# Optimization experiments

Measured on AMD Instinct MI355X. Metric: run time of the kernel, lower is better.

The kernel has to match this reference:

```python
import jax, jax.numpy as jnp
import numpy as np

HEADS, DIM_KEY, DIM_VALUE, DIM, N, B = 8, 64, 192, 1536, 2048, 2
SCALE = DIM_KEY ** -0.5


def setup_inputs() -> dict:
    key = jax.random.key(0)
    ks = jax.random.split(key, 8)
    s = 0.02
    return {
        "x": jax.random.normal(ks[0], (B, N, DIM), jnp.float32),
        "Wq": jax.random.normal(ks[1], (DIM, HEADS * DIM_KEY), jnp.float32) * s,
        "Wk": jax.random.normal(ks[2], (DIM, HEADS * DIM_KEY), jnp.float32) * s,
        "Wv": jax.random.normal(ks[3], (DIM, HEADS * DIM_VALUE), jnp.float32) * s,
        "Wo": jax.random.normal(ks[4], (HEADS * DIM_VALUE, DIM), jnp.float32) * s,
        "bo": jnp.zeros((DIM,), jnp.float32),
        "pos_embed": jax.random.normal(ks[5], (HEADS, N, DIM_KEY), jnp.float32) * s,
        "rel_content_bias": jax.random.normal(ks[6], (1, HEADS, 1, DIM_KEY), jnp.float32),
    }


def _split_heads(t, d):
    # [B, N, H*d] -> [B, H, N, d]
    b, n, _ = t.shape
    return t.reshape(b, n, HEADS, d).transpose(0, 2, 1, 3)


def reference(x, Wq, Wk, Wv, Wo, bo, pos_embed, rel_content_bias):
    q = _split_heads(x @ Wq, DIM_KEY) * SCALE          # [B,H,N,dk]
    k = _split_heads(x @ Wk, DIM_KEY)                  # [B,H,N,dk]
    v = _split_heads(x @ Wv, DIM_VALUE)                # [B,H,N,dv]
    q_biased = q + pos_embed[None] + rel_content_bias  # additive biases fused into Q
    logits = jnp.einsum('bhid,bhjd->bhij', q_biased, k)
    attn = jax.nn.softmax(logits, axis=-1)
    out = jnp.einsum('bhij,bhjd->bhid', attn, v)       # [B,H,N,dv]
    out = out.transpose(0, 2, 1, 3).reshape(x.shape[0], x.shape[1], HEADS * DIM_VALUE)
    return out @ Wo + bo
```

## Files before the change

### kernel.cpp

```cpp
#include <hip/hip_runtime.h>

#define BB    2
#define HN    8
#define NSEQ  2048
#define DIMM  1536
#define DKD   64
#define DVD   192
#define QCOLS 512
#define VCOLS 1536

typedef short short8 __attribute__((ext_vector_type(8)));
typedef float f32x4  __attribute__((ext_vector_type(4)));
typedef unsigned short ushortT;

static __device__ inline ushortT f2bf(float f) {
    unsigned u = __builtin_bit_cast(unsigned, f);
    u = (u + 0x7FFFu + ((u >> 16) & 1u)) >> 16;
    return (ushortT)u;
}

static __device__ inline void gl_lds16(const ushortT* g, ushortT* l) {
    __builtin_amdgcn_global_load_lds(
        (const __attribute__((address_space(1))) unsigned int*)g,
        (__attribute__((address_space(3))) unsigned int*)l, 16, 0, 0);
}

#define FENCE_VM0()    asm volatile("s_waitcnt vmcnt(0)" ::: "memory")
#define FENCE_VM12()   asm volatile("s_waitcnt vmcnt(12)" ::: "memory")
#define FENCE_LGKM0()  asm volatile("s_waitcnt lgkmcnt(0)" ::: "memory")
#define FENCE_SOFT()   asm volatile("" ::: "memory")

__global__ __launch_bounds__(256)
void prep_kernel(const float* __restrict__ x,
                 const float* __restrict__ Wq, const float* __restrict__ Wk,
                 const float* __restrict__ Wv, const float* __restrict__ Wo,
                 ushortT* __restrict__ xb, ushortT* __restrict__ wqkv,
                 ushortT* __restrict__ wo_t)
{
    __shared__ ushortT tt[32][33];
    const int b = blockIdx.x, tid = threadIdx.x;

    if (b < 3072) {
        const size_t idx = (size_t)b * 256 + tid;
        const float4* p = (const float4*)x + idx * 2;
        const float4 a = p[0], c = p[1];
        short8 v;
        v[0] = f2bf(a.x); v[1] = f2bf(a.y); v[2] = f2bf(a.z); v[3] = f2bf(a.w);
        v[4] = f2bf(c.x); v[5] = f2bf(c.y); v[6] = f2bf(c.z); v[7] = f2bf(c.w);
        *(short8*)(xb + idx * 8) = v;
        return;
    }

    const float* W; ushortT* Wt; int ncols, t;
    if (b < 3840)      { W = Wq; Wt = wqkv;                          ncols = QCOLS; t = b - 3072; }
    else if (b < 4608) { W = Wk; Wt = wqkv + (size_t)QCOLS * DIMM;   ncols = QCOLS; t = b - 3840; }
    else if (b < 6912) { W = Wv; Wt = wqkv + (size_t)2*QCOLS * DIMM; ncols = VCOLS; t = b - 4608; }
    else               { W = Wo; Wt = wo_t;                          ncols = DIMM;  t = b - 6912; }

    const int nbx = ncols >> 5;
    const int c0 = (t % nbx) * 32, k0 = (t / nbx) * 32;
    const int lx = tid & 31, ly = tid >> 5;
    #pragma unroll
    for (int r = 0; r < 4; r++)
        tt[ly + r * 8][lx] = f2bf(W[(size_t)(k0 + ly + r * 8) * ncols + c0 + lx]);
    __syncthreads();
    #pragma unroll
    for (int r = 0; r < 4; r++)
        Wt[(size_t)(c0 + ly + r * 8) * DIMM + k0 + lx] = tt[lx][ly + r * 8];
}

__global__ __launch_bounds__(256)
void gemm_kernel(const ushortT* __restrict__ A, const ushortT* __restrict__ Bt,
                 const float* __restrict__ bo,
                 const float* __restrict__ pos, const float* __restrict__ rcb,
                 ushortT* __restrict__ q_ws, ushortT* __restrict__ k_ws,
                 ushortT* __restrict__ v_ws, float* __restrict__ Cout, int mode)
{
    __shared__ ushortT As[128 * 64];
    __shared__ ushortT Bs[64 * 64];

    const int tid  = threadIdx.x;
    const int wave = tid >> 6, lane = tid & 63;
    const int quad = lane >> 4, l15 = lane & 15;
    const int m0 = blockIdx.y * 128, n0 = blockIdx.x * 64;

    const int sl_r = lane >> 3;
    const int sl_c = ((lane & 7) ^ sl_r) * 8;

    const ushortT* Ab = A  + (size_t)m0 * DIMM;
    const ushortT* Bb = Bt + (size_t)n0 * DIMM;

    f32x4 acc[2][4];
    #pragma unroll
    for (int i = 0; i < 2; i++)
        #pragma unroll
        for (int j = 0; j < 4; j++) acc[i][j] = (f32x4){0.f, 0.f, 0.f, 0.f};

    for (int k0 = 0; k0 < DIMM; k0 += 64) {
        #pragma unroll
        for (int t = 0; t < 4; t++) {
            const int g = wave * 4 + t;
            gl_lds16(Ab + (size_t)(g * 8 + sl_r) * DIMM + k0 + sl_c, &As[g * 512]);
        }
        #pragma unroll
        for (int t = 0; t < 2; t++) {
            const int g = wave * 2 + t;
            gl_lds16(Bb + (size_t)(g * 8 + sl_r) * DIMM + k0 + sl_c, &Bs[g * 512]);
        }
        __syncthreads();

        short8 af[2][2], bf[4][2];
        #pragma unroll
        for (int i = 0; i < 2; i++) {
            const int r = wave * 32 + i * 16 + l15;
            #pragma unroll
            for (int ks = 0; ks < 2; ks++)
                af[i][ks] = *(const short8*)&As[r * 64 + ((ks * 4 + quad) ^ (l15 & 7)) * 8];
        }
        #pragma unroll
        for (int j = 0; j < 4; j++) {
            const int r = j * 16 + l15;
            #pragma unroll
            for (int ks = 0; ks < 2; ks++)
                bf[j][ks] = *(const short8*)&Bs[r * 64 + ((ks * 4 + quad) ^ (l15 & 7)) * 8];
        }

        #pragma unroll
        for (int ks = 0; ks < 2; ks++)
            #pragma unroll
            for (int i = 0; i < 2; i++)
                #pragma unroll
                for (int j = 0; j < 4; j++)
                    acc[i][j] = __builtin_amdgcn_mfma_f32_16x16x32_bf16(af[i][ks], bf[j][ks], acc[i][j], 0, 0, 0);

        __syncthreads();
    }

    #pragma unroll
    for (int i = 0; i < 2; i++) {
        #pragma unroll
        for (int j = 0; j < 4; j++) {
            const int gcol = n0 + j * 16 + l15;
            #pragma unroll
            for (int r = 0; r < 4; r++) {
                const int grow = m0 + wave * 32 + i * 16 + quad * 4 + r;
                const float val = acc[i][j][r];
                if (mode == 1) {
                    Cout[(size_t)grow * DIMM + gcol] = val + bo[gcol];
                } else {
                    const int b = grow >> 11, n = grow & (NSEQ - 1);
                    if (gcol < QCOLS) {
                        const int h = gcol >> 6, d = gcol & 63;
                        q_ws[((size_t)(b * HN + h) * NSEQ + n) * DKD + d] =
                            f2bf(val * 0.125f + pos[((size_t)h * NSEQ + n) * DKD + d] + rcb[h * DKD + d]);
                    } else if (gcol < 2 * QCOLS) {
                        const int c = gcol - QCOLS, h = c >> 6, d = c & 63;
                        k_ws[((size_t)(b * HN + h) * NSEQ + n) * DKD + d] = f2bf(val);
                    } else {
                        const int c = gcol - 2 * QCOLS, h = c / DVD, d = c - h * DVD;
                        v_ws[((size_t)(b * HN + h) * DVD + d) * NSEQ + n] = f2bf(val);
                    }
                }
            }
        }
    }
}

#define PLD2 40
#define SHIFT 20.0f

__global__ __launch_bounds__(128)
void flash_kernel(const ushortT* __restrict__ q_ws, const ushortT* __restrict__ k_ws,
                  const ushortT* __restrict__ v_ws, ushortT* __restrict__ attn)
{
    __shared__ ushortT lds[16384 + 2 * 32 * PLD2];

    const int tid = threadIdx.x;
    const int wave = tid >> 6, lane = tid & 63;
    const int quad = lane >> 4, l15 = lane & 15;

    const int bh = blockIdx.x & 15;
    const int qt = blockIdx.x >> 4;
    const int n0 = qt * 32;
    const int b  = bh >> 3, h = bh & 7;

    const ushortT* kg = k_ws + (size_t)bh * NSEQ * DKD + (size_t)(wave * 1024) * DKD;
    const ushortT* vg = v_ws + (size_t)bh * DVD * NSEQ + wave * 1024;

    ushortT* st = lds + wave * 8192;
    ushortT* Pw = lds + 16384 + wave * (32 * PLD2);

    const int k_r = lane >> 3, k_c = ((lane & 7) ^ (k_r & 7)) * 8;
    const int v_r = lane >> 2, v_c = ((lane & 3) ^ (v_r & 3)) * 8;

    short8 qf[2][2];
    #pragma unroll
    for (int mt = 0; mt < 2; mt++)
        #pragma unroll
        for (int ks = 0; ks < 2; ks++)
            qf[mt][ks] = *(const short8*)(q_ws + ((size_t)bh * NSEQ + n0 + mt * 16 + l15) * DKD + ks * 32 + quad * 8);

    f32x4 o[2][12];
    #pragma unroll
    for (int mt = 0; mt < 2; mt++)
        #pragma unroll
        for (int nt = 0; nt < 12; nt++) o[mt][nt] = (f32x4){0.f, 0.f, 0.f, 0.f};

    float l_part[2][4];
    #pragma unroll
    for (int mt = 0; mt < 2; mt++)
        #pragma unroll
        for (int i = 0; i < 4; i++) l_part[mt][i] = 0.f;

    for (int kt0 = 0; kt0 < 1024; kt0 += 32) {
        FENCE_LGKM0();

        #pragma unroll
        for (int t = 0; t < 4; t++)
            gl_lds16(kg + (size_t)(kt0 + t * 8 + k_r) * DKD + k_c, st + t * 512);
        #pragma unroll
        for (int u = 0; u < 12; u++)
            gl_lds16(vg + (size_t)(u * 16 + v_r) * NSEQ + kt0 + v_c, st + 2048 + u * 512);

        FENCE_VM12();

        f32x4 s[2][2];
        #pragma unroll
        for (int mt = 0; mt < 2; mt++)
            #pragma unroll
            for (int nt = 0; nt < 2; nt++) s[mt][nt] = (f32x4){0.f, 0.f, 0.f, 0.f};
        #pragma unroll
        for (int ks = 0; ks < 2; ks++)
            #pragma unroll
            for (int nt = 0; nt < 2; nt++) {
                const int key = nt * 16 + l15;
                short8 kf = *(const short8*)&st[key * 64 + (((ks * 4 + quad) ^ (key & 7)) * 8)];
                s[0][nt] = __builtin_amdgcn_mfma_f32_16x16x32_bf16(qf[0][ks], kf, s[0][nt], 0, 0, 0);
                s[1][nt] = __builtin_amdgcn_mfma_f32_16x16x32_bf16(qf[1][ks], kf, s[1][nt], 0, 0, 0);
            }

        #pragma unroll
        for (int mt = 0; mt < 2; mt++)
            #pragma unroll
            for (int nt = 0; nt < 2; nt++)
                #pragma unroll
                for (int i = 0; i < 4; i++) {
                    const float p = __expf(s[mt][nt][i] - SHIFT);
                    s[mt][nt][i] = p;
                    l_part[mt][i] += p;
                    Pw[(mt * 16 + quad * 4 + i) * PLD2 + nt * 16 + l15] = f2bf(p);
                }

        FENCE_SOFT();

        short8 a[2];
        #pragma unroll
        for (int mt = 0; mt < 2; mt++)
            a[mt] = *(const short8*)&Pw[(mt * 16 + l15) * PLD2 + quad * 8];

        FENCE_VM0();

        #pragma unroll
        for (int nt2 = 0; nt2 < 12; nt2++) {
            const int d = nt2 * 16 + l15;
            short8 vf = *(const short8*)&st[2048 + d * 32 + ((quad ^ (d & 3)) * 8)];
            o[0][nt2] = __builtin_amdgcn_mfma_f32_16x16x32_bf16(a[0], vf, o[0][nt2], 0, 0, 0);
            o[1][nt2] = __builtin_amdgcn_mfma_f32_16x16x32_bf16(a[1], vf, o[1][nt2], 0, 0, 0);
        }
    }

    #pragma unroll
    for (int off = 1; off <= 8; off <<= 1)
        #pragma unroll
        for (int mt = 0; mt < 2; mt++)
            #pragma unroll
            for (int i = 0; i < 4; i++)
                l_part[mt][i] += __shfl_xor(l_part[mt][i], off, 64);

    __syncthreads();
    float* ox = (float*)lds;
    float* lx = (float*)(lds + 16384);
    if (wave == 1) {
        #pragma unroll
        for (int mt = 0; mt < 2; mt++)
            #pragma unroll
            for (int nt2 = 0; nt2 < 12; nt2++)
                #pragma unroll
                for (int i = 0; i < 4; i++)
                    ox[(((mt * 12 + nt2) * 4 + i) * 64) + lane] = o[mt][nt2][i];
        #pragma unroll
        for (int mt = 0; mt < 2; mt++)
            #pragma unroll
            for (int i = 0; i < 4; i++)
                lx[(mt * 4 + i) * 64 + lane] = l_part[mt][i];
    }
    __syncthreads();
    if (wave == 0) {
        float inv[2][4];
        #pragma unroll
        for (int mt = 0; mt < 2; mt++)
            #pragma unroll
            for (int i = 0; i < 4; i++)
                inv[mt][i] = 1.f / (l_part[mt][i] + lx[(mt * 4 + i) * 64 + lane]);
        #pragma unroll
        for (int mt = 0; mt < 2; mt++)
            #pragma unroll
            for (int nt2 = 0; nt2 < 12; nt2++)
                #pragma unroll
                for (int i = 0; i < 4; i++) {
                    const float v = o[mt][nt2][i] + ox[(((mt * 12 + nt2) * 4 + i) * 64) + lane];
                    const int n = n0 + mt * 16 + quad * 4 + i;
                    attn[((size_t)b * NSEQ + n) * DIMM + h * DVD + nt2 * 16 + l15] =
                        f2bf(v * inv[mt][i]);
                }
    }
}

extern "C" void kernel_launch(void* const* d_in, const int* in_sizes, int n_in,
                              void* d_out, int out_size, void* d_ws, size_t ws_size,
                              hipStream_t stream)
{
    const float* x   = (const float*)d_in[0];
    const float* Wq  = (const float*)d_in[1];
    const float* Wk  = (const float*)d_in[2];
    const float* Wv  = (const float*)d_in[3];
    const float* Wo  = (const float*)d_in[4];
    const float* bo  = (const float*)d_in[5];
    const float* pos = (const float*)d_in[6];
    const float* rcb = (const float*)d_in[7];
    float* out = (float*)d_out;

    ushortT* xb    = (ushortT*)d_ws;
    ushortT* wqkv  = xb    + (size_t)4096 * DIMM;
    ushortT* wo_t  = wqkv  + (size_t)(2 * QCOLS + VCOLS) * DIMM;
    ushortT* q_ws  = wo_t  + (size_t)DIMM * DIMM;
    ushortT* k_ws  = q_ws  + (size_t)BB * HN * NSEQ * DKD;
    ushortT* v_ws  = k_ws  + (size_t)BB * HN * NSEQ * DKD;
    ushortT* attnb = v_ws  + (size_t)BB * HN * NSEQ * DVD;

    prep_kernel<<<dim3(9216), dim3(256), 0, stream>>>(x, Wq, Wk, Wv, Wo, xb, wqkv, wo_t);

    gemm_kernel<<<dim3(40, 32), dim3(256), 0, stream>>>(xb, wqkv, bo, pos, rcb,
                                                        q_ws, k_ws, v_ws, nullptr, 0);
    flash_kernel<<<dim3(1024), dim3(128), 0, stream>>>(q_ws, k_ws, v_ws, attnb);
    gemm_kernel<<<dim3(24, 32), dim3(256), 0, stream>>>(attnb, wo_t, bo, pos, rcb,
                                                        q_ws, k_ws, v_ws, out, 1);
}
```

Baseline: 261.0 us.

## Triple-buffer GEMM K-loop with BK=32 and pack P via v_cvt_pk_bf16 with permuted V

The projection GEMM moves from a single-buffered BK=64 loop with two __syncthreads per step to a three-stage ring of BK=32 tiles. Global-to-LDS loads for step kt+2 are issued before computing step kt, with vmcnt waits and one barrier per step, so load latency overlaps the MFMAs. In the attention kernel, pairs of exp results are converted with v_cvt_pk_bf16_f32 and written to LDS as one 32-bit store. This needs V's sequence index permuted within each 32-key group, which the GEMM epilogue does when writing v_ws. The changes add complexity around the wait counts and the coupled P/V layout, and the smaller K tile halves MFMA work per barrier.

```diff
diff --git a/kernel.cpp b/kernel.cpp
--- a/kernel.cpp
+++ b/kernel.cpp
@@ -26,6 +26,7 @@
 }
 
 #define FENCE_VM0()    asm volatile("s_waitcnt vmcnt(0)" ::: "memory")
+#define FENCE_VM3()    asm volatile("s_waitcnt vmcnt(3)" ::: "memory")
 #define FENCE_VM12()   asm volatile("s_waitcnt vmcnt(12)" ::: "memory")
 #define FENCE_LGKM0()  asm volatile("s_waitcnt lgkmcnt(0)" ::: "memory")
 #define FENCE_SOFT()   asm volatile("" ::: "memory")
@@ -69,6 +70,9 @@
         Wt[(size_t)(c0 + ly + r * 8) * DIMM + k0 + lx] = tt[lx][ly + r * 8];
 }
 
+#define BKG   32
+#define NKT3  (DIMM / BKG)
+
 __global__ __launch_bounds__(256)
 void gemm_kernel(const ushortT* __restrict__ A, const ushortT* __restrict__ Bt,
                  const float* __restrict__ bo,
@@ -76,16 +80,16 @@
                  ushortT* __restrict__ q_ws, ushortT* __restrict__ k_ws,
                  ushortT* __restrict__ v_ws, float* __restrict__ Cout, int mode)
 {
-    __shared__ ushortT As[128 * 64];
-    __shared__ ushortT Bs[64 * 64];
+    __shared__ ushortT As[3][128 * BKG];
+    __shared__ ushortT Bs[3][64 * BKG];
 
     const int tid  = threadIdx.x;
     const int wave = tid >> 6, lane = tid & 63;
     const int quad = lane >> 4, l15 = lane & 15;
     const int m0 = blockIdx.y * 128, n0 = blockIdx.x * 64;
 
-    const int sl_r = lane >> 3;
-    const int sl_c = ((lane & 7) ^ sl_r) * 8;
+    const int sl_r = lane >> 2;
+    const int sl_c = ((lane & 3) ^ (sl_r & 3)) * 8;
 
     const ushortT* Ab = A  + (size_t)m0 * DIMM;
     const ushortT* Bb = Bt + (size_t)n0 * DIMM;
@@ -96,44 +100,47 @@
         #pragma unroll
         for (int j = 0; j < 4; j++) acc[i][j] = (f32x4){0.f, 0.f, 0.f, 0.f};
 
-    for (int k0 = 0; k0 < DIMM; k0 += 64) {
-        #pragma unroll
-        for (int t = 0; t < 4; t++) {
-            const int g = wave * 4 + t;
-            gl_lds16(Ab + (size_t)(g * 8 + sl_r) * DIMM + k0 + sl_c, &As[g * 512]);
-        }
-        #pragma unroll
-        for (int t = 0; t < 2; t++) {
-            const int g = wave * 2 + t;
-            gl_lds16(Bb + (size_t)(g * 8 + sl_r) * DIMM + k0 + sl_c, &Bs[g * 512]);
-        }
-        __syncthreads();
-
-        short8 af[2][2], bf[4][2];
+    auto STAGE = [&](int t) {
+        const int k0 = t * BKG;
+        const int bf3 = t % 3;
+        #pragma unroll
+        for (int u = 0; u < 2; u++) {
+            const int g = wave * 2 + u;
+            gl_lds16(Ab + (size_t)(g * 16 + sl_r) * DIMM + k0 + sl_c, &As[bf3][g * 512]);
+        }
+        gl_lds16(Bb + (size_t)(wave * 16 + sl_r) * DIMM + k0 + sl_c, &Bs[bf3][wave * 512]);
+    };
+
+    STAGE(0);
+    STAGE(1);
+    FENCE_VM3();
+    __builtin_amdgcn_s_barrier();
+
+    for (int kt = 0; kt < NKT3; kt++) {
+        if (kt + 2 < NKT3) STAGE(kt + 2);
+
+        const int bf3 = kt % 3;
+        short8 af[2], bf[4];
         #pragma unroll
         for (int i = 0; i < 2; i++) {
             const int r = wave * 32 + i * 16 + l15;
-            #pragma unroll
-            for (int ks = 0; ks < 2; ks++)
-                af[i][ks] = *(const short8*)&As[r * 64 + ((ks * 4 + quad) ^ (l15 & 7)) * 8];
+            af[i] = *(const short8*)&As[bf3][r * BKG + ((quad ^ (r & 3)) * 8)];
         }
         #pragma unroll
         for (int j = 0; j < 4; j++) {
             const int r = j * 16 + l15;
-            #pragma unroll
-            for (int ks = 0; ks < 2; ks++)
-                bf[j][ks] = *(const short8*)&Bs[r * 64 + ((ks * 4 + quad) ^ (l15 & 7)) * 8];
-        }
-
-        #pragma unroll
-        for (int ks = 0; ks < 2; ks++)
-            #pragma unroll
-            for (int i = 0; i < 2; i++)
-                #pragma unroll
-                for (int j = 0; j < 4; j++)
-                    acc[i][j] = __builtin_amdgcn_mfma_f32_16x16x32_bf16(af[i][ks], bf[j][ks], acc[i][j], 0, 0, 0);
-
-        __syncthreads();
+            bf[j] = *(const short8*)&Bs[bf3][r * BKG + ((quad ^ (r & 3)) * 8)];
+        }
+
+        #pragma unroll
+        for (int i = 0; i < 2; i++)
+            #pragma unroll
+            for (int j = 0; j < 4; j++)
+                acc[i][j] = __builtin_amdgcn_mfma_f32_16x16x32_bf16(af[i], bf[j], acc[i][j], 0, 0, 0);
+
+        if (kt + 2 < NKT3)      { FENCE_VM3(); }
+        else if (kt + 1 < NKT3) { FENCE_VM0(); }
+        __builtin_amdgcn_s_barrier();
     }
 
     #pragma unroll
@@ -158,7 +165,8 @@
                         k_ws[((size_t)(b * HN + h) * NSEQ + n) * DKD + d] = f2bf(val);
                     } else {
                         const int c = gcol - 2 * QCOLS, h = c / DVD, d = c - h * DVD;
-                        v_ws[((size_t)(b * HN + h) * DVD + d) * NSEQ + n] = f2bf(val);
+                        const int p = (n & ~31) | (((n & 15) << 1) | ((n >> 4) & 1));
+                        v_ws[((size_t)(b * HN + h) * DVD + d) * NSEQ + p] = f2bf(val);
                     }
                 }
             }
@@ -242,14 +250,14 @@
         #pragma unroll
         for (int mt = 0; mt < 2; mt++)
             #pragma unroll
-            for (int nt = 0; nt < 2; nt++)
-                #pragma unroll
-                for (int i = 0; i < 4; i++) {
-                    const float p = __expf(s[mt][nt][i] - SHIFT);
-                    s[mt][nt][i] = p;
-                    l_part[mt][i] += p;
-                    Pw[(mt * 16 + quad * 4 + i) * PLD2 + nt * 16 + l15] = f2bf(p);
-                }
+            for (int i = 0; i < 4; i++) {
+                const float p0 = __expf(s[mt][0][i] - SHIFT);
+                const float p1 = __expf(s[mt][1][i] - SHIFT);
+                l_part[mt][i] += p0 + p1;
+                unsigned pk;
+                asm("v_cvt_pk_bf16_f32 %0, %1, %2" : "=v"(pk) : "v"(p0), "v"(p1));
+                *(unsigned*)&Pw[(mt * 16 + quad * 4 + i) * PLD2 + 2 * l15] = pk;
+            }
 
         FENCE_SOFT();
 
```

After: 295.2 us. 1.13x slower.
